# Kernel tuning notes

Hardware: AMD Instinct MI355X
Metric: run time of the kernel (lower is better)

Reference implementation:

```python
import jax, jax.numpy as jnp
import numpy as np

IMG = 32
CX = CY = IMG // 2
B = 65536


def setup_inputs() -> dict:
    key = jax.random.key(0)
    k1, k2, k3 = jax.random.split(key, 3)
    W = jax.random.normal(k1, (B, 16), dtype=jnp.float32)
    noise_randn = jax.random.normal(k2, (B, IMG, IMG), dtype=jnp.float32)
    noise_rand = jax.random.uniform(k3, (B, IMG, IMG), dtype=jnp.float32)
    return {"W": W, "noise_randn": noise_randn, "noise_rand": noise_rand}


def reference(W, noise_randn, noise_rand):
    H = IMG
    PI = jnp.float32(np.pi)
    ar = jnp.arange(H, dtype=jnp.float32)
    xx, yy = jnp.meshgrid(ar, ar, indexing="ij")  # (H, H)

    def c(k):  # per-sample scalar broadcast to (B,1,1)
        return W[:, k][:, None, None]

    r = jnp.sqrt((xx - CX) ** 2 + (yy - CY) ** 2)  # (H, H)

    # layer 0: clipped radial cone
    img = jnp.clip(c(0) * 5 - r, 0.0, 1.0)
    # layer 1: centered square (torch int(clamp(...).item()) == floor for positive vals)
    half = jnp.floor(jnp.clip(jnp.abs(c(1)) * 8, 2.0, 12.0))
    mask1 = ((xx >= CY - half) & (xx < CY + half) & (yy >= CX - half) & (yy < CX + half))
    img = img + 0.5 * mask1.astype(jnp.float32)
    # layers 2-4: sinusoids
    img = img + 0.5 * jnp.sin(c(2) * 10 * PI * xx / H)
    img = img + 0.5 * jnp.sin(c(3) * 10 * PI * yy / H)
    img = img + 0.5 * jnp.sin(c(4) * 5 * PI * (xx + yy) / (2 * H))
    # layer 5: warp
    img = img + 0.5 * jnp.sin((yy + c(5) * 10) * PI / H)
    # layer 6: bias
    img = img + c(6)
    # layer 7: gaussian blob; int() truncates toward zero
    bx = jnp.trunc(CX + c(7) * 5)
    by = jnp.trunc(CY + c(7) * 5)
    sigma = 4.0 + jnp.abs(c(7)) * 4.0
    img = img + jnp.exp(-((xx - bx) ** 2 + (yy - by) ** 2) / (2 * sigma ** 2))
    # layer 8: ring
    img = img + ((r - c(8) * 10) ** 2 < 10.0).astype(jnp.float32)
    # layer 9: checkerboard; cb_size = int(clamp(|w|*8+2, 2, 16)) -> floor
    cb = jnp.floor(jnp.clip(jnp.abs(c(9)) * 8 + 2, 2.0, 16.0))
    img = img + jnp.mod(jnp.floor(xx / cb) + jnp.floor(yy / cb), 2.0) * 0.3
    # layer 10: rotated line
    angle = c(10) * PI
    rot_line = jnp.cos(angle) * (xx - CX) + jnp.sin(angle) * (yy - CY)
    img = img + (jnp.abs(rot_line) < 3.0).astype(jnp.float32) * 0.6
    # layer 11: angular sinusoid
    theta = jnp.arctan2(yy - CY, xx - CX)
    img = img + 0.5 * jnp.sin(theta * c(11) * 5)
    # layers 12-13: noise (deterministic inputs replace randn_like/rand_like)
    img = img + noise_randn * 0.1 * c(12)
    img = img + (noise_rand - 0.5) * c(13) * 0.05
    # layer 14: contrast
    img = (img - 0.5) * (1.0 + c(14)) + 0.5
    # layer 15: conditional inversion
    img = jnp.where(c(15) > 0, 1.0 - img, img)
    # per-image min-max normalize
    mn = jnp.min(img, axis=(1, 2), keepdims=True)
    mx = jnp.max(img, axis=(1, 2), keepdims=True)
    img = (img - mn) / (mx - mn + 1e-8)
    return img[:, None, :, :]  # (B, 1, H, W)
```

## Files before the change

kernel.cpp:

```cpp
#include <hip/hip_runtime.h>
#include <math.h>

#define NB 65536
#define IMGD 32
#define NPIX 1024
#define PSTRIDE 20

typedef float v2f __attribute__((ext_vector_type(2)));

#define PK_FMA(d, a, b, c) \
    asm("v_pk_fma_f32 %0, %1, %2, %3" : "=v"(d) : "v"(a), "v"(b), "v"(c))
#define PK_FMA_CLAMP(d, a, b, c) \
    asm("v_pk_fma_f32 %0, %1, %2, %3 clamp" : "=v"(d) : "v"(a), "v"(b), "v"(c))
#define PK_FMA_ACC(acc, a, b) \
    asm("v_pk_fma_f32 %0, %1, %2, %0" : "+v"(acc) : "v"(a), "v"(b))
#define PK_ADD(d, a, b) \
    asm("v_pk_add_f32 %0, %1, %2" : "=v"(d) : "v"(a), "v"(b))
#define PK_ADD_ACC(acc, a) \
    asm("v_pk_add_f32 %0, %0, %1" : "+v"(acc) : "v"(a))
#define PK_MUL(d, a, b) \
    asm("v_pk_mul_f32 %0, %1, %2" : "=v"(d) : "v"(a), "v"(b))

__device__ __align__(16) float g_r[NPIX];
__device__ __align__(16) float g_th[NPIX];
__device__ __align__(16) float g_par[(size_t)NB * PSTRIDE];

__global__ void init_params_kernel(const float* __restrict__ W) {
    int b = blockIdx.x * blockDim.x + threadIdx.x;

    if (blockIdx.x == 0) {
        int t = threadIdx.x;
        for (int k = 0; k < 4; ++k) {
            int p = t * 4 + k;
            int x = p >> 5, y = p & 31;
            float dx = (float)(x - 16), dy = (float)(y - 16);
            g_r[p] = sqrtf(dx * dx + dy * dy);
            g_th[p] = atan2f(dy, dx) * 0.79577471545947668f;
        }
    }
    if (b >= NB) return;
    const float* w = W + (size_t)b * 16;
    float* P = g_par + (size_t)b * PSTRIDE;

    float w0 = w[0], w1 = w[1], w2 = w[2], w3 = w[3], w4 = w[4], w5 = w[5],
          w6 = w[6], w7 = w[7], w8 = w[8], w9 = w[9], w10 = w[10], w11 = w[11],
          w12 = w[12], w13 = w[13], w14 = w[14], w15 = w[15];

    P[0] = w0 * 5.0f;
    float half = floorf(fminf(fmaxf(fabsf(w1) * 8.0f, 2.0f), 12.0f));
    P[1] = 16.0f - half;
    P[2] = 16.0f + half;
    P[3] = w2 * 0.15625f;
    P[4] = w3 * 0.15625f;
    P[5] = w4 * 0.0390625f;
    P[6] = w5 * 0.15625f;
    P[7] = w6;
    float t7 = __fadd_rn(16.0f, __fmul_rn(w7, 5.0f));
    P[8] = truncf(t7);
    float sg = 4.0f + fabsf(w7) * 4.0f;
    P[9] = -1.0f / (2.0f * sg * sg);
    P[10] = w8 * 10.0f;
    float cb = floorf(fminf(fmaxf(__fadd_rn(fabsf(w9) * 8.0f, 2.0f), 2.0f), 16.0f));
    P[11] = cb;
    P[12] = 1.0f / cb;
    float ang = __fmul_rn(w10, 3.14159265358979323846f);
    P[13] = (float)cos((double)ang);
    P[14] = (float)sin((double)ang);
    P[15] = w11;
    P[16] = w12 * 0.1f;
    P[17] = w13 * 0.05f;
    P[18] = 1.0f + w14;
    P[19] = w15;
}

__device__ __forceinline__ float hsin(float rev) {
    return __builtin_amdgcn_sinf(__builtin_amdgcn_fractf(rev));
}

__device__ __forceinline__ float fdivq(float xf, float cb, float rcb) {
    float q = floorf(xf * rcb);
    q += ((q + 1.0f) * cb <= xf) ? 1.0f : 0.0f;
    q -= ((q * cb) > xf) ? 1.0f : 0.0f;
    return q;
}

template <int CTRL>
__device__ __forceinline__ float dpp_step_min(float v) {
    int i = __float_as_int(v);
    int s = __builtin_amdgcn_update_dpp(i, i, CTRL, 0xf, 0xf, false);
    return fminf(v, __int_as_float(s));
}
template <int CTRL>
__device__ __forceinline__ float dpp_step_max(float v) {
    int i = __float_as_int(v);
    int s = __builtin_amdgcn_update_dpp(i, i, CTRL, 0xf, 0xf, false);
    return fmaxf(v, __int_as_float(s));
}

__global__ __launch_bounds__(256) void decode_kernel(
        const float* __restrict__ nrand,
        const float* __restrict__ nunif,
        float* __restrict__ out) {
    int b = blockIdx.x;
    int t = threadIdx.x;

    const float4* Pq = (const float4*)(g_par + (size_t)b * PSTRIDE);
    float4 q0 = Pq[0], q1 = Pq[1], q2 = Pq[2], q3 = Pq[3], q4 = Pq[4];
    float a0 = q0.x, lo = q0.y, hi = q0.z, s2 = q0.w;
    float s3 = q1.x, s4 = q1.y, s5o = q1.z, w6 = q1.w;
    float bxy = q2.x, nk = q2.y, t8 = q2.z, cb = q2.w;
    float rcb = q3.x, ca = q3.y, sa = q3.z, w11 = q3.w;
    float k12 = q4.x, k13 = q4.y, con = q4.z, w15 = q4.w;

    __shared__ float4 xt4[32];
    __shared__ float  rx[32];
    __shared__ float  ysum[32];
    __shared__ float  ym05[32];
    __shared__ float  pyt[32];
    __shared__ float  gyt[32];
    __shared__ float  syt[32];
    __shared__ float  stab[63];

    if (t < 32) {
        float xf = (float)t;
        float qx = fdivq(xf, cb, rcb);
        float px = qx - 2.0f * floorf(qx * 0.5f);
        float d  = xf - bxy;
        float4 e;
        e.x = 0.5f * hsin(s2 * xf) + 0.3f * px;
        e.y = (xf >= lo && xf < hi) ? 1.0f : 0.0f;
        e.z = -0.6f * px;
        e.w = __expf(d * d * nk);
        xt4[t] = e;
        rx[t] = __fmul_rn(ca, xf - 16.0f);
    } else if (t < 64) {
        int   y  = t - 32;
        float yf = (float)y;
        float qy = fdivq(yf, cb, rcb);
        float py = qy - 2.0f * floorf(qy * 0.5f);
        float d  = yf - bxy;
        ysum[y] = 0.5f * hsin(s3 * yf) + 0.5f * hsin(0.015625f * yf + s5o)
                  + 0.3f * py + w6 - 0.5f * k13;
        ym05[y] = (yf >= lo && yf < hi) ? 0.5f : 0.0f;
        pyt[y]  = py;
        gyt[y]  = __expf(d * d * nk);
        syt[y]  = __fmul_rn(sa, yf - 16.0f);
    } else if (t < 127) {
        int s = t - 64;
        stab[s] = 0.5f * hsin(s4 * (float)s);
    }
    __syncthreads();

    int x  = t >> 3;
    int y0 = (t & 7) * 4;

    float4 X   = xt4[x];
    float  rxv = rx[x];

    v2f ysA = *(const v2f*)&ysum[y0], ysB = *(const v2f*)&ysum[y0 + 2];
    v2f ymA = *(const v2f*)&ym05[y0], ymB = *(const v2f*)&ym05[y0 + 2];
    v2f pyA = *(const v2f*)&pyt[y0],  pyB = *(const v2f*)&pyt[y0 + 2];
    v2f gyA = *(const v2f*)&gyt[y0],  gyB = *(const v2f*)&gyt[y0 + 2];
    v2f syA = *(const v2f*)&syt[y0],  syB = *(const v2f*)&syt[y0 + 2];
    int s0 = x + y0;
    v2f stA = {stab[s0], stab[s0 + 1]}, stB = {stab[s0 + 2], stab[s0 + 3]};

    size_t q = (size_t)b * 256 + (size_t)t;
    float4 R  = ((const float4*)g_r)[t];
    float4 TH = ((const float4*)g_th)[t];
    float4 NR = ((const float4*)nrand)[q];
    float4 NU = ((const float4*)nunif)[q];

    const v2f m1   = {-1.0f, -1.0f};
    const v2f a02  = {a0, a0};
    const v2f xs2  = {X.x, X.x};
    const v2f xm2  = {X.y, X.y};
    const v2f px2  = {X.z, X.z};
    const v2f gx2  = {X.w, X.w};
    const v2f rx2  = {rxv, rxv};
    const v2f nt82 = {-t8, -t8};
    const v2f w112 = {w11, w11};
    const v2f h2   = {0.5f, 0.5f};
    const v2f k122 = {k12, k12};
    const v2f k132 = {k13, k13};

    v2f i01, i23;
    float mn, mx;

#pragma unroll
    for (int k = 0; k < 2; ++k) {
        v2f r2  = k ? (v2f){R.z, R.w}   : (v2f){R.x, R.y};
        v2f th2 = k ? (v2f){TH.z, TH.w} : (v2f){TH.x, TH.y};
        v2f nr2 = k ? (v2f){NR.z, NR.w} : (v2f){NR.x, NR.y};
        v2f nu2 = k ? (v2f){NU.z, NU.w} : (v2f){NU.x, NU.y};
        v2f ys = k ? ysB : ysA, ym = k ? ymB : ymA, py = k ? pyB : pyA;
        v2f gy = k ? gyB : gyA, sy = k ? syB : syA, st = k ? stB : stA;

        v2f v;
        PK_FMA_CLAMP(v, r2, m1, a02);
        PK_ADD_ACC(v, ys);
        PK_ADD_ACC(v, xs2);
        PK_ADD_ACC(v, st);
        PK_FMA_ACC(v, xm2, ym);
        PK_FMA_ACC(v, px2, py);
        PK_FMA_ACC(v, gx2, gy);
        v2f dr, dr2, rot, ang;
        PK_ADD(dr, r2, nt82);
        PK_MUL(dr2, dr, dr);
        PK_ADD(rot, sy, rx2);
        PK_MUL(ang, th2, w112);
        v2f sn = {hsin(ang.x), hsin(ang.y)};
        PK_FMA_ACC(v, sn, h2);
        PK_FMA_ACC(v, nr2, k122);
        PK_FMA_ACC(v, nu2, k132);

        float vx = v.x + ((dr2.x < 10.0f) ? 1.0f : 0.0f);
        float vy = v.y + ((dr2.y < 10.0f) ? 1.0f : 0.0f);
        vx += (fabsf(rot.x) < 3.0f) ? 0.6f : 0.0f;
        vy += (fabsf(rot.y) < 3.0f) ? 0.6f : 0.0f;

        v2f r_ = {vx, vy};
        if (k == 0) { i01 = r_; mn = fminf(vx, vy); mx = fmaxf(vx, vy); }
        else        { i23 = r_; mn = fminf(mn, fminf(vx, vy));
                                mx = fmaxf(mx, fmaxf(vx, vy)); }
    }

    mn = dpp_step_min<0x111>(mn);
    mx = dpp_step_max<0x111>(mx);
    mn = dpp_step_min<0x112>(mn);
    mx = dpp_step_max<0x112>(mx);
    mn = dpp_step_min<0x114>(mn);
    mx = dpp_step_max<0x114>(mx);
    mn = dpp_step_min<0x118>(mn);
    mx = dpp_step_max<0x118>(mx);
    mn = dpp_step_min<0x142>(mn);
    mx = dpp_step_max<0x142>(mx);
    mn = dpp_step_min<0x143>(mn);
    mx = dpp_step_max<0x143>(mx);
    mn = __int_as_float(__builtin_amdgcn_readlane(__float_as_int(mn), 63));
    mx = __int_as_float(__builtin_amdgcn_readlane(__float_as_int(mx), 63));

    __shared__ float smn[4], smx[4];
    int wid = t >> 6;
    if ((t & 63) == 0) { smn[wid] = mn; smx[wid] = mx; }
    __syncthreads();
    mn = fminf(fminf(smn[0], smn[1]), fminf(smn[2], smn[3]));
    mx = fmaxf(fmaxf(smx[0], smx[1]), fmaxf(smx[2], smx[3]));

    float ac    = fabsf(con);
    float denom = fmaf(ac, mx - mn, 1e-8f);
    float s     = ac / denom;
    bool  eff   = (w15 > 0.0f) != (con < 0.0f);
    float bse   = eff ? mx : mn;
    float sgn   = eff ? -s : s;
    v2f c12 = {sgn, sgn};
    v2f c02 = {-bse * sgn, -bse * sgn};

    v2f o01, o23;
    PK_FMA(o01, i01, c12, c02);
    PK_FMA(o23, i23, c12, c02);
    float4 O = {o01.x, o01.y, o23.x, o23.y};
    ((float4*)out)[q] = O;
}

extern "C" void kernel_launch(void* const* d_in, const int* in_sizes, int n_in,
                              void* d_out, int out_size, void* d_ws, size_t ws_size,
                              hipStream_t stream) {
    const float* W  = (const float*)d_in[0];
    const float* nr = (const float*)d_in[1];
    const float* nu = (const float*)d_in[2];
    float* out = (float*)d_out;

    init_params_kernel<<<NB / 256, 256, 0, stream>>>(W);
    decode_kernel<<<NB, 256, 0, stream>>>(nr, nu, out);
}
```

Measured before the change: 146.5 us.

## Compute per-row/column tables in registers instead of shared memory, drop barrier

Each thread now computes the x-dependent and four y-dependent terms it needs directly in registers, replacing the shared-memory tables built by the first 127 threads and the __syncthreads barrier. The global loads of radius, angle and noise are issued at kernel start so their latency overlaps this setup math. The cost is redundant transcendental work: every thread runs several hsin and exp calls instead of one, which raises ALU load and register pressure.

```diff
diff --git a/kernel.cpp b/kernel.cpp
--- a/kernel.cpp
+++ b/kernel.cpp
@@ -104,6 +104,12 @@
     int b = blockIdx.x;
     int t = threadIdx.x;
 
+    size_t q = (size_t)b * 256 + (size_t)t;
+    float4 R  = ((const float4*)g_r)[t];
+    float4 TH = ((const float4*)g_th)[t];
+    float4 NR = ((const float4*)nrand)[q];
+    float4 NU = ((const float4*)nunif)[q];
+
     const float4* Pq = (const float4*)(g_par + (size_t)b * PSTRIDE);
     float4 q0 = Pq[0], q1 = Pq[1], q2 = Pq[2], q3 = Pq[3], q4 = Pq[4];
     float a0 = q0.x, lo = q0.y, hi = q0.z, s2 = q0.w;
@@ -112,71 +118,49 @@
     float rcb = q3.x, ca = q3.y, sa = q3.z, w11 = q3.w;
     float k12 = q4.x, k13 = q4.y, con = q4.z, w15 = q4.w;
 
-    __shared__ float4 xt4[32];
-    __shared__ float  rx[32];
-    __shared__ float  ysum[32];
-    __shared__ float  ym05[32];
-    __shared__ float  pyt[32];
-    __shared__ float  gyt[32];
-    __shared__ float  syt[32];
-    __shared__ float  stab[63];
-
-    if (t < 32) {
-        float xf = (float)t;
-        float qx = fdivq(xf, cb, rcb);
-        float px = qx - 2.0f * floorf(qx * 0.5f);
-        float d  = xf - bxy;
-        float4 e;
-        e.x = 0.5f * hsin(s2 * xf) + 0.3f * px;
-        e.y = (xf >= lo && xf < hi) ? 1.0f : 0.0f;
-        e.z = -0.6f * px;
-        e.w = __expf(d * d * nk);
-        xt4[t] = e;
-        rx[t] = __fmul_rn(ca, xf - 16.0f);
-    } else if (t < 64) {
-        int   y  = t - 32;
+    int x  = t >> 3;
+    int y0 = (t & 7) * 4;
+    float xf = (float)x;
+
+    float qx   = fdivq(xf, cb, rcb);
+    float px   = qx - 2.0f * floorf(qx * 0.5f);
+    float dxx  = xf - bxy;
+    float xsum = 0.5f * hsin(s2 * xf) + 0.3f * px;
+    float xmv  = (xf >= lo && xf < hi) ? 1.0f : 0.0f;
+    float mpx  = -0.6f * px;
+    float gx   = __expf(dxx * dxx * nk);
+    float rxv  = __fmul_rn(ca, xf - 16.0f);
+
+    float ysv[4], ymv[4], pyv[4], gyv[4], syv[4], stv[4];
+#pragma unroll
+    for (int i = 0; i < 4; ++i) {
+        int   y  = y0 + i;
         float yf = (float)y;
         float qy = fdivq(yf, cb, rcb);
         float py = qy - 2.0f * floorf(qy * 0.5f);
         float d  = yf - bxy;
-        ysum[y] = 0.5f * hsin(s3 * yf) + 0.5f * hsin(0.015625f * yf + s5o)
-                  + 0.3f * py + w6 - 0.5f * k13;
-        ym05[y] = (yf >= lo && yf < hi) ? 0.5f : 0.0f;
-        pyt[y]  = py;
-        gyt[y]  = __expf(d * d * nk);
-        syt[y]  = __fmul_rn(sa, yf - 16.0f);
-    } else if (t < 127) {
-        int s = t - 64;
-        stab[s] = 0.5f * hsin(s4 * (float)s);
+        ysv[i] = 0.5f * hsin(s3 * yf) + 0.5f * hsin(0.015625f * yf + s5o)
+                 + 0.3f * py + w6 - 0.5f * k13;
+        ymv[i] = (yf >= lo && yf < hi) ? 0.5f : 0.0f;
+        pyv[i] = py;
+        gyv[i] = __expf(d * d * nk);
+        syv[i] = __fmul_rn(sa, yf - 16.0f);
+        stv[i] = 0.5f * hsin(s4 * (float)(x + y));
     }
-    __syncthreads();
-
-    int x  = t >> 3;
-    int y0 = (t & 7) * 4;
-
-    float4 X   = xt4[x];
-    float  rxv = rx[x];
-
-    v2f ysA = *(const v2f*)&ysum[y0], ysB = *(const v2f*)&ysum[y0 + 2];
-    v2f ymA = *(const v2f*)&ym05[y0], ymB = *(const v2f*)&ym05[y0 + 2];
-    v2f pyA = *(const v2f*)&pyt[y0],  pyB = *(const v2f*)&pyt[y0 + 2];
-    v2f gyA = *(const v2f*)&gyt[y0],  gyB = *(const v2f*)&gyt[y0 + 2];
-    v2f syA = *(const v2f*)&syt[y0],  syB = *(const v2f*)&syt[y0 + 2];
-    int s0 = x + y0;
-    v2f stA = {stab[s0], stab[s0 + 1]}, stB = {stab[s0 + 2], stab[s0 + 3]};
-
-    size_t q = (size_t)b * 256 + (size_t)t;
-    float4 R  = ((const float4*)g_r)[t];
-    float4 TH = ((const float4*)g_th)[t];
-    float4 NR = ((const float4*)nrand)[q];
-    float4 NU = ((const float4*)nunif)[q];
+
+    v2f ysA = {ysv[0], ysv[1]}, ysB = {ysv[2], ysv[3]};
+    v2f ymA = {ymv[0], ymv[1]}, ymB = {ymv[2], ymv[3]};
+    v2f pyA = {pyv[0], pyv[1]}, pyB = {pyv[2], pyv[3]};
+    v2f gyA = {gyv[0], gyv[1]}, gyB = {gyv[2], gyv[3]};
+    v2f syA = {syv[0], syv[1]}, syB = {syv[2], syv[3]};
+    v2f stA = {stv[0], stv[1]}, stB = {stv[2], stv[3]};
 
     const v2f m1   = {-1.0f, -1.0f};
     const v2f a02  = {a0, a0};
-    const v2f xs2  = {X.x, X.x};
-    const v2f xm2  = {X.y, X.y};
-    const v2f px2  = {X.z, X.z};
-    const v2f gx2  = {X.w, X.w};
+    const v2f xs2  = {xsum, xsum};
+    const v2f xm2  = {xmv, xmv};
+    const v2f px2  = {mpx, mpx};
+    const v2f gx2  = {gx, gx};
     const v2f rx2  = {rxv, rxv};
     const v2f nt82 = {-t8, -t8};
     const v2f w112 = {w11, w11};
```

Result: slower. 169.2 us (+15.5%).

## Process eight images per block with double-buffered tables and prefetched noise

Applied to the files above, without the earlier changes.

Each block now handles eight images in sequence rather than one. The per-image lookup tables go into a double-buffered LDS area, and the next image's noise loads and parameters are prefetched while the current image is computed. The aim is to cut block launch overhead, reuse the radius and angle loads, and hide global memory latency. In exchange there are fewer blocks in flight (8192) and a serial dependency chain inside each block, which may lower memory-level parallelism for what is a bandwidth-bound kernel.

```diff
diff --git a/kernel.cpp b/kernel.cpp
--- a/kernel.cpp
+++ b/kernel.cpp
@@ -2,9 +2,10 @@
 #include <math.h>
 
 #define NB 65536
-#define IMGD 32
 #define NPIX 1024
 #define PSTRIDE 20
+#define IPB 8
+#define NBLK (NB / IPB)
 
 typedef float v2f __attribute__((ext_vector_type(2)));
 
@@ -97,29 +98,13 @@
     return fmaxf(v, __int_as_float(s));
 }
 
-__global__ __launch_bounds__(256) void decode_kernel(
-        const float* __restrict__ nrand,
-        const float* __restrict__ nunif,
-        float* __restrict__ out) {
-    int b = blockIdx.x;
-    int t = threadIdx.x;
-
-    const float4* Pq = (const float4*)(g_par + (size_t)b * PSTRIDE);
-    float4 q0 = Pq[0], q1 = Pq[1], q2 = Pq[2], q3 = Pq[3], q4 = Pq[4];
-    float a0 = q0.x, lo = q0.y, hi = q0.z, s2 = q0.w;
+__device__ __forceinline__ void table_setup(float* __restrict__ L, int t,
+        float4 q0, float4 q1, float4 q2, float4 q3, float4 q4) {
+    float lo = q0.y, hi = q0.z, s2 = q0.w;
     float s3 = q1.x, s4 = q1.y, s5o = q1.z, w6 = q1.w;
-    float bxy = q2.x, nk = q2.y, t8 = q2.z, cb = q2.w;
-    float rcb = q3.x, ca = q3.y, sa = q3.z, w11 = q3.w;
-    float k12 = q4.x, k13 = q4.y, con = q4.z, w15 = q4.w;
-
-    __shared__ float4 xt4[32];
-    __shared__ float  rx[32];
-    __shared__ float  ysum[32];
-    __shared__ float  ym05[32];
-    __shared__ float  pyt[32];
-    __shared__ float  gyt[32];
-    __shared__ float  syt[32];
-    __shared__ float  stab[63];
+    float bxy = q2.x, nk = q2.y, cb = q2.w;
+    float rcb = q3.x, ca = q3.y, sa = q3.z;
+    float k13 = q4.y;
 
     if (t < 32) {
         float xf = (float)t;
@@ -131,136 +116,182 @@
         e.y = (xf >= lo && xf < hi) ? 1.0f : 0.0f;
         e.z = -0.6f * px;
         e.w = __expf(d * d * nk);
-        xt4[t] = e;
-        rx[t] = __fmul_rn(ca, xf - 16.0f);
+        ((float4*)L)[t] = e;
+        L[128 + t] = __fmul_rn(ca, xf - 16.0f);
     } else if (t < 64) {
         int   y  = t - 32;
         float yf = (float)y;
         float qy = fdivq(yf, cb, rcb);
         float py = qy - 2.0f * floorf(qy * 0.5f);
         float d  = yf - bxy;
-        ysum[y] = 0.5f * hsin(s3 * yf) + 0.5f * hsin(0.015625f * yf + s5o)
-                  + 0.3f * py + w6 - 0.5f * k13;
-        ym05[y] = (yf >= lo && yf < hi) ? 0.5f : 0.0f;
-        pyt[y]  = py;
-        gyt[y]  = __expf(d * d * nk);
-        syt[y]  = __fmul_rn(sa, yf - 16.0f);
+        L[160 + y] = 0.5f * hsin(s3 * yf) + 0.5f * hsin(0.015625f * yf + s5o)
+                     + 0.3f * py + w6 - 0.5f * k13;
+        L[192 + y] = (yf >= lo && yf < hi) ? 0.5f : 0.0f;
+        L[224 + y] = py;
+        L[256 + y] = __expf(d * d * nk);
+        L[288 + y] = __fmul_rn(sa, yf - 16.0f);
     } else if (t < 127) {
         int s = t - 64;
-        stab[s] = 0.5f * hsin(s4 * (float)s);
+        L[320 + s] = 0.5f * hsin(s4 * (float)s);
     }
-    __syncthreads();
+}
+
+__global__ __launch_bounds__(256) void decode_kernel(
+        const float* __restrict__ nrand,
+        const float* __restrict__ nunif,
+        float* __restrict__ out) {
+    int t = threadIdx.x;
+    int base = blockIdx.x * IPB;
 
     int x  = t >> 3;
     int y0 = (t & 7) * 4;
 
-    float4 X   = xt4[x];
-    float  rxv = rx[x];
-
-    v2f ysA = *(const v2f*)&ysum[y0], ysB = *(const v2f*)&ysum[y0 + 2];
-    v2f ymA = *(const v2f*)&ym05[y0], ymB = *(const v2f*)&ym05[y0 + 2];
-    v2f pyA = *(const v2f*)&pyt[y0],  pyB = *(const v2f*)&pyt[y0 + 2];
-    v2f gyA = *(const v2f*)&gyt[y0],  gyB = *(const v2f*)&gyt[y0 + 2];
-    v2f syA = *(const v2f*)&syt[y0],  syB = *(const v2f*)&syt[y0 + 2];
-    int s0 = x + y0;
-    v2f stA = {stab[s0], stab[s0 + 1]}, stB = {stab[s0 + 2], stab[s0 + 3]};
-
-    size_t q = (size_t)b * 256 + (size_t)t;
-    float4 R  = ((const float4*)g_r)[t];
-    float4 TH = ((const float4*)g_th)[t];
-    float4 NR = ((const float4*)nrand)[q];
-    float4 NU = ((const float4*)nunif)[q];
-
-    const v2f m1   = {-1.0f, -1.0f};
-    const v2f a02  = {a0, a0};
-    const v2f xs2  = {X.x, X.x};
-    const v2f xm2  = {X.y, X.y};
-    const v2f px2  = {X.z, X.z};
-    const v2f gx2  = {X.w, X.w};
-    const v2f rx2  = {rxv, rxv};
-    const v2f nt82 = {-t8, -t8};
-    const v2f w112 = {w11, w11};
-    const v2f h2   = {0.5f, 0.5f};
-    const v2f k122 = {k12, k12};
-    const v2f k132 = {k13, k13};
-
-    v2f i01, i23;
-    float mn, mx;
+    float4 Rr  = ((const float4*)g_r)[t];
+    float4 THr = ((const float4*)g_th)[t];
+
+    __shared__ __align__(16) float lds[2][384];
+    __shared__ float smn[4], smx[4];
+
+    float4 c0, c1, c2, c3, c4, n0, n1, n2, n3, n4;
+    {
+        const float4* P = (const float4*)(g_par + (size_t)base * PSTRIDE);
+        c0 = P[0]; c1 = P[1]; c2 = P[2]; c3 = P[3]; c4 = P[4];
+        const float4* Q = (const float4*)(g_par + (size_t)(base + 1) * PSTRIDE);
+        n0 = Q[0]; n1 = Q[1]; n2 = Q[2]; n3 = Q[3]; n4 = Q[4];
+    }
+    size_t qi = (size_t)base * 256 + (size_t)t;
+    float4 NRc = ((const float4*)nrand)[qi];
+    float4 NUc = ((const float4*)nunif)[qi];
+
+    table_setup(&lds[0][0], t, c0, c1, c2, c3, c4);
+    __syncthreads();
+
+    int cur = 0;
+#pragma unroll 1
+    for (int i = 0; i < IPB; ++i) {
+        bool more = (i + 1 < IPB);
+        float4 NRn, NUn;
+        if (more) {
+            size_t qn = (size_t)(base + i + 1) * 256 + (size_t)t;
+            NRn = ((const float4*)nrand)[qn];
+            NUn = ((const float4*)nunif)[qn];
+            table_setup(&lds[cur ^ 1][0], t, n0, n1, n2, n3, n4);
+        }
+
+        const float* L = &lds[cur][0];
+        float a0 = c0.x, t8 = c2.z, w11 = c3.w;
+        float k12 = c4.x, k13 = c4.y, con = c4.z, w15 = c4.w;
+
+        float4 X   = *(const float4*)&L[4 * x];
+        float  rxv = L[128 + x];
+        v2f ysA = *(const v2f*)&L[160 + y0], ysB = *(const v2f*)&L[160 + y0 + 2];
+        v2f ymA = *(const v2f*)&L[192 + y0], ymB = *(const v2f*)&L[192 + y0 + 2];
+        v2f pyA = *(const v2f*)&L[224 + y0], pyB = *(const v2f*)&L[224 + y0 + 2];
+        v2f gyA = *(const v2f*)&L[256 + y0], gyB = *(const v2f*)&L[256 + y0 + 2];
+        v2f syA = *(const v2f*)&L[288 + y0], syB = *(const v2f*)&L[288 + y0 + 2];
+        int s0 = x + y0;
+        v2f stA = {L[320 + s0], L[320 + s0 + 1]};
+        v2f stB = {L[320 + s0 + 2], L[320 + s0 + 3]};
+
+        const v2f m1   = {-1.0f, -1.0f};
+        const v2f a02  = {a0, a0};
+        const v2f xs2  = {X.x, X.x};
+        const v2f xm2  = {X.y, X.y};
+        const v2f px2  = {X.z, X.z};
+        const v2f gx2  = {X.w, X.w};
+        const v2f rx2  = {rxv, rxv};
+        const v2f nt82 = {-t8, -t8};
+        const v2f w112 = {w11, w11};
+        const v2f h2   = {0.5f, 0.5f};
+        const v2f k122 = {k12, k12};
+        const v2f k132 = {k13, k13};
+
+        v2f i01, i23;
+        float mn, mx;
 
 #pragma unroll
-    for (int k = 0; k < 2; ++k) {
-        v2f r2  = k ? (v2f){R.z, R.w}   : (v2f){R.x, R.y};
-        v2f th2 = k ? (v2f){TH.z, TH.w} : (v2f){TH.x, TH.y};
-        v2f nr2 = k ? (v2f){NR.z, NR.w} : (v2f){NR.x, NR.y};
-        v2f nu2 = k ? (v2f){NU.z, NU.w} : (v2f){NU.x, NU.y};
-        v2f ys = k ? ysB : ysA, ym = k ? ymB : ymA, py = k ? pyB : pyA;
-        v2f gy = k ? gyB : gyA, sy = k ? syB : syA, st = k ? stB : stA;
-
-        v2f v;
-        PK_FMA_CLAMP(v, r2, m1, a02);
-        PK_ADD_ACC(v, ys);
-        PK_ADD_ACC(v, xs2);
-        PK_ADD_ACC(v, st);
-        PK_FMA_ACC(v, xm2, ym);
-        PK_FMA_ACC(v, px2, py);
-        PK_FMA_ACC(v, gx2, gy);
-        v2f dr, dr2, rot, ang;
-        PK_ADD(dr, r2, nt82);
-        PK_MUL(dr2, dr, dr);
-        PK_ADD(rot, sy, rx2);
-        PK_MUL(ang, th2, w112);
-        v2f sn = {hsin(ang.x), hsin(ang.y)};
-        PK_FMA_ACC(v, sn, h2);
-        PK_FMA_ACC(v, nr2, k122);
-        PK_FMA_ACC(v, nu2, k132);
-
-        float vx = v.x + ((dr2.x < 10.0f) ? 1.0f : 0.0f);
-        float vy = v.y + ((dr2.y < 10.0f) ? 1.0f : 0.0f);
-        vx += (fabsf(rot.x) < 3.0f) ? 0.6f : 0.0f;
-        vy += (fabsf(rot.y) < 3.0f) ? 0.6f : 0.0f;
-
-        v2f r_ = {vx, vy};
-        if (k == 0) { i01 = r_; mn = fminf(vx, vy); mx = fmaxf(vx, vy); }
-        else        { i23 = r_; mn = fminf(mn, fminf(vx, vy));
-                                mx = fmaxf(mx, fmaxf(vx, vy)); }
+        for (int k = 0; k < 2; ++k) {
+            v2f r2  = k ? (v2f){Rr.z, Rr.w}   : (v2f){Rr.x, Rr.y};
+            v2f th2 = k ? (v2f){THr.z, THr.w} : (v2f){THr.x, THr.y};
+            v2f nr2 = k ? (v2f){NRc.z, NRc.w} : (v2f){NRc.x, NRc.y};
+            v2f nu2 = k ? (v2f){NUc.z, NUc.w} : (v2f){NUc.x, NUc.y};
+            v2f ys = k ? ysB : ysA, ym = k ? ymB : ymA, py = k ? pyB : pyA;
+            v2f gy = k ? gyB : gyA, sy = k ? syB : syA, st = k ? stB : stA;
+
+            v2f v;
+            PK_FMA_CLAMP(v, r2, m1, a02);
+            PK_ADD_ACC(v, ys);
+            PK_ADD_ACC(v, xs2);
+            PK_ADD_ACC(v, st);
+            PK_FMA_ACC(v, xm2, ym);
+            PK_FMA_ACC(v, px2, py);
+            PK_FMA_ACC(v, gx2, gy);
+            v2f dr, dr2, rot, ang;
+            PK_ADD(dr, r2, nt82);
+            PK_MUL(dr2, dr, dr);
+            PK_ADD(rot, sy, rx2);
+            PK_MUL(ang, th2, w112);
+            v2f sn = {hsin(ang.x), hsin(ang.y)};
+            PK_FMA_ACC(v, sn, h2);
+            PK_FMA_ACC(v, nr2, k122);
+            PK_FMA_ACC(v, nu2, k132);
+
+            float vx = v.x + ((dr2.x < 10.0f) ? 1.0f : 0.0f);
+            float vy = v.y + ((dr2.y < 10.0f) ? 1.0f : 0.0f);
+            vx += (fabsf(rot.x) < 3.0f) ? 0.6f : 0.0f;
+            vy += (fabsf(rot.y) < 3.0f) ? 0.6f : 0.0f;
+
+            v2f r_ = {vx, vy};
+            if (k == 0) { i01 = r_; mn = fminf(vx, vy); mx = fmaxf(vx, vy); }
+            else        { i23 = r_; mn = fminf(mn, fminf(vx, vy));
+                                    mx = fmaxf(mx, fmaxf(vx, vy)); }
+        }
+
+        mn = dpp_step_min<0x111>(mn);  mx = dpp_step_max<0x111>(mx);
+        mn = dpp_step_min<0x112>(mn);  mx = dpp_step_max<0x112>(mx);
+        mn = dpp_step_min<0x114>(mn);  mx = dpp_step_max<0x114>(mx);
+        mn = dpp_step_min<0x118>(mn);  mx = dpp_step_max<0x118>(mx);
+        mn = dpp_step_min<0x142>(mn);  mx = dpp_step_max<0x142>(mx);
+        mn = dpp_step_min<0x143>(mn);  mx = dpp_step_max<0x143>(mx);
+        mn = __int_as_float(__builtin_amdgcn_readlane(__float_as_int(mn), 63));
+        mx = __int_as_float(__builtin_amdgcn_readlane(__float_as_int(mx), 63));
+
+        int wid = t >> 6;
+        if ((t & 63) == 0) { smn[wid] = mn; smx[wid] = mx; }
+        __syncthreads();
+        mn = fminf(fminf(smn[0], smn[1]), fminf(smn[2], smn[3]));
+        mx = fmaxf(fmaxf(smx[0], smx[1]), fmaxf(smx[2], smx[3]));
+
+        float ac    = fabsf(con);
+        float denom = fmaf(ac, mx - mn, 1e-8f);
+        float s     = ac / denom;
+        bool  eff   = (w15 > 0.0f) != (con < 0.0f);
+        float bse   = eff ? mx : mn;
+        float sgn   = eff ? -s : s;
+        v2f c12 = {sgn, sgn};
+        v2f c02 = {-bse * sgn, -bse * sgn};
+
+        v2f o01, o23;
+        PK_FMA(o01, i01, c12, c02);
+        PK_FMA(o23, i23, c12, c02);
+        float4 O = {o01.x, o01.y, o23.x, o23.y};
+        ((float4*)out)[(size_t)(base + i) * 256 + (size_t)t] = O;
+
+        float4 m0, m1q, m2, m3, m4;
+        bool more2 = (i + 2 < IPB);
+        if (more2) {
+            const float4* M =
+                (const float4*)(g_par + (size_t)(base + i + 2) * PSTRIDE);
+            m0 = M[0]; m1q = M[1]; m2 = M[2]; m3 = M[3]; m4 = M[4];
+        }
+        __syncthreads();
+        if (more) {
+            c0 = n0; c1 = n1; c2 = n2; c3 = n3; c4 = n4;
+            NRc = NRn; NUc = NUn;
+            if (more2) { n0 = m0; n1 = m1q; n2 = m2; n3 = m3; n4 = m4; }
+            cur ^= 1;
+        }
     }
-
-    mn = dpp_step_min<0x111>(mn);
-    mx = dpp_step_max<0x111>(mx);
-    mn = dpp_step_min<0x112>(mn);
-    mx = dpp_step_max<0x112>(mx);
-    mn = dpp_step_min<0x114>(mn);
-    mx = dpp_step_max<0x114>(mx);
-    mn = dpp_step_min<0x118>(mn);
-    mx = dpp_step_max<0x118>(mx);
-    mn = dpp_step_min<0x142>(mn);
-    mx = dpp_step_max<0x142>(mx);
-    mn = dpp_step_min<0x143>(mn);
-    mx = dpp_step_max<0x143>(mx);
-    mn = __int_as_float(__builtin_amdgcn_readlane(__float_as_int(mn), 63));
-    mx = __int_as_float(__builtin_amdgcn_readlane(__float_as_int(mx), 63));
-
-    __shared__ float smn[4], smx[4];
-    int wid = t >> 6;
-    if ((t & 63) == 0) { smn[wid] = mn; smx[wid] = mx; }
-    __syncthreads();
-    mn = fminf(fminf(smn[0], smn[1]), fminf(smn[2], smn[3]));
-    mx = fmaxf(fmaxf(smx[0], smx[1]), fmaxf(smx[2], smx[3]));
-
-    float ac    = fabsf(con);
-    float denom = fmaf(ac, mx - mn, 1e-8f);
-    float s     = ac / denom;
-    bool  eff   = (w15 > 0.0f) != (con < 0.0f);
-    float bse   = eff ? mx : mn;
-    float sgn   = eff ? -s : s;
-    v2f c12 = {sgn, sgn};
-    v2f c02 = {-bse * sgn, -bse * sgn};
-
-    v2f o01, o23;
-    PK_FMA(o01, i01, c12, c02);
-    PK_FMA(o23, i23, c12, c02);
-    float4 O = {o01.x, o01.y, o23.x, o23.y};
-    ((float4*)out)[q] = O;
 }
 
 extern "C" void kernel_launch(void* const* d_in, const int* in_sizes, int n_in,
@@ -272,5 +303,5 @@
     float* out = (float*)d_out;
 
     init_params_kernel<<<NB / 256, 256, 0, stream>>>(W);
-    decode_kernel<<<NB, 256, 0, stream>>>(nr, nu, out);
-}
+    decode_kernel<<<NBLK, 256, 0, stream>>>(nr, nu, out);
+}
```

Measured after the change: 160.3 us. +9.4%, slower.
